# Kernel optimization log

Hardware: AMD Instinct MI355X
Metric: run time of the kernel (lower is better)

The kernel has to match this reference:

```python
import jax, jax.numpy as jnp
import numpy as np

D_MODEL = 4096
N_CHUNKS = 8
CHUNK = D_MODEL // N_CHUNKS
EPS = 1e-5


def setup_inputs() -> dict:
    key = jax.random.key(0)
    k = jax.random.split(key, 5)
    B, L = 4, 4096
    x = jax.random.normal(k[0], (B, L, D_MODEL), dtype=jnp.float32)
    # kaiming_uniform with a=sqrt(5) on [n,c,c]: fan_in = c, bound = 1/sqrt(fan_in)
    bound = 1.0 / np.sqrt(CHUNK)
    w1 = jax.random.uniform(k[1], (N_CHUNKS, CHUNK, CHUNK), jnp.float32, -bound, bound)
    w2 = jax.random.uniform(k[2], (N_CHUNKS, CHUNK, CHUNK), jnp.float32, -bound, bound)
    b1 = jnp.zeros((N_CHUNKS, CHUNK), jnp.float32)
    b2 = jnp.zeros((N_CHUNKS, CHUNK), jnp.float32)
    ln_g = jnp.ones((D_MODEL,), jnp.float32)
    ln_b = jnp.zeros((D_MODEL,), jnp.float32)
    return {"x": x, "w1": w1, "b1": b1, "w2": w2, "b2": b2, "ln_g": ln_g, "ln_b": ln_b}


def reference(x, w1, b1, w2, b2, ln_g, ln_b):
    B, L, d = x.shape
    xc = x.reshape(B, L, N_CHUNKS, CHUNK)
    h = jnp.einsum('blnc,ncd->blnd', xc, w1) + b1
    h = jax.nn.gelu(h, approximate=False)  # torch F.gelu default is exact erf
    h = jnp.einsum('blnc,ncd->blnd', h, w2) + b2
    out = h.reshape(B, L, d) + x  # dropout p=0.0 -> identity
    mu = jnp.mean(out, axis=-1, keepdims=True)
    var = jnp.var(out, axis=-1, keepdims=True)
    return (out - mu) * jax.lax.rsqrt(var + EPS) * ln_g + ln_b
```

## Files before the change

### kernel.cpp

```cpp
#include <hip/hip_runtime.h>
#include <hip/hip_bf16.h>

#define TOKENS 16384
#define DMODEL 4096
#define NCH 8
#define CH 512
#define BM 64

typedef short s16x8 __attribute__((ext_vector_type(8)));
typedef float f32x4 __attribute__((ext_vector_type(4)));

__device__ __forceinline__ unsigned short f2bf(float f) {
    unsigned u = __float_as_uint(f);
    u += 0x7fffu + ((u >> 16) & 1u);
    return (unsigned short)(u >> 16);
}

__device__ __forceinline__ float gelu_fast(float x) {
    float u = 1.5957691216057308f * x * (1.0f + 0.044715f * x * x);
    float e = __expf(u);
    return x - x * __builtin_amdgcn_rcpf(e + 1.0f);
}

__global__ __launch_bounds__(256)
void wprep_kernel(const float* __restrict__ w1, const float* __restrict__ w2,
                  unsigned short* __restrict__ p1, unsigned short* __restrict__ p2)
{
    const int lane = threadIdx.x;
    const int sub  = threadIdx.y;
    const int kt   = blockIdx.x;
    const int nb   = blockIdx.y * 4 + sub;
    const int which = blockIdx.z >> 3;
    const int n     = blockIdx.z & 7;

    const int kg  = lane >> 4;
    const int l15 = lane & 15;

    const float* src = (which ? w2 : w1) + (size_t)n * CH * CH;
    unsigned short* dst = (which ? p2 : p1) + (size_t)n * CH * CH
                        + ((size_t)(kt * 32 + nb) * 64 + lane) * 8;

    unsigned short v[8];
#pragma unroll
    for (int j = 0; j < 8; ++j)
        v[j] = f2bf(src[(size_t)(kt * 32 + kg * 8 + j) * CH + nb * 16 + l15]);

    uint4 q;
    q.x = (unsigned)v[0] | ((unsigned)v[1] << 16);
    q.y = (unsigned)v[2] | ((unsigned)v[3] << 16);
    q.z = (unsigned)v[4] | ((unsigned)v[5] << 16);
    q.w = (unsigned)v[6] | ((unsigned)v[7] << 16);
    *(uint4*)dst = q;
}

#define XC_BYTES (BM * CH * 2)
#define BBUF(i)  (XC_BYTES + (i) * 32768)

__global__ __launch_bounds__(512, 1)
void mlp_kernel(const float* __restrict__ x,
                const unsigned short* __restrict__ p1,
                const unsigned short* __restrict__ p2,
                const float* __restrict__ b1,
                const float* __restrict__ b2,
                float* __restrict__ mid)
{
    __shared__ unsigned char lds[XC_BYTES + 3 * 32768];
    const int tile = blockIdx.x;
    const int n    = blockIdx.y;
    const int tid  = threadIdx.x;
    const int wid  = tid >> 6;
    const int lane = tid & 63;
    const int row0 = tile * BM;
    const int kt0  = (tile >> 3) & 15;

    const unsigned short* p1n = p1 + (size_t)n * CH * CH;
    const unsigned short* p2n = p2 + (size_t)n * CH * CH;

    const int nwoff = wid * 64;
    const int l15   = lane & 15;
    const int kg    = lane >> 4;

    float b1v[4], b2v[4];
#pragma unroll
    for (int ni = 0; ni < 4; ++ni) {
        int col = n * CH + nwoff + ni * 16 + l15;
        b1v[ni] = b1[col];
        b2v[ni] = b2[col];
    }

    auto stageB = [&](const unsigned short* pk, int kt, int bufb) {
#pragma unroll
        for (int i = 0; i < 4; ++i) {
            const unsigned short* src = pk + ((size_t)(kt * 32 + wid * 4 + i) * 64 + lane) * 8;
            unsigned char* dstp = lds + bufb + (wid * 4 + i) * 1024;
            __builtin_amdgcn_global_load_lds(
                (const __attribute__((address_space(1))) void*)src,
                (__attribute__((address_space(3))) void*)dstp,
                16, 0, 0);
        }
    };

    stageB(p1n, kt0, BBUF(0));
    stageB(p1n, (kt0 + 1) & 15, BBUF(1));
    {
        const float* xc = x + (size_t)row0 * DMODEL + n * CH;
#pragma unroll
        for (int it = 0; it < 16; ++it) {
            int f = it * 512 + tid;
            int r = f >> 7;
            int c = (f & 127) << 2;
            const float4 v = *(const float4*)(xc + (size_t)r * DMODEL + c);
            unsigned lo = (unsigned)f2bf(v.x) | ((unsigned)f2bf(v.y) << 16);
            unsigned hi = (unsigned)f2bf(v.z) | ((unsigned)f2bf(v.w) << 16);
            int byte = ((r * CH + c) * 2) ^ ((r & 7) << 4);
            *(uint2*)(lds + byte) = make_uint2(lo, hi);
        }
    }
    __syncthreads();

    f32x4 acc[4][4];
    auto zacc = [&]() {
#pragma unroll
        for (int mi = 0; mi < 4; ++mi)
#pragma unroll
            for (int ni = 0; ni < 4; ++ni)
                acc[mi][ni] = (f32x4){0.f, 0.f, 0.f, 0.f};
    };

    auto step = [&](int kt, int bufb) {
        s16x8 a[4], b[4];
#pragma unroll
        for (int mi = 0; mi < 4; ++mi) {
            int r = mi * 16 + l15;
            int byte = ((r * CH + kt * 32 + kg * 8) * 2) ^ ((r & 7) << 4);
            a[mi] = *(const s16x8*)(lds + byte);
        }
#pragma unroll
        for (int ni = 0; ni < 4; ++ni)
            b[ni] = *(const s16x8*)(lds + bufb + ((wid * 4 + ni) * 64 + lane) * 16);
#pragma unroll
        for (int ni = 0; ni < 4; ++ni)
#pragma unroll
            for (int mi = 0; mi < 4; ++mi)
                acc[mi][ni] = __builtin_amdgcn_mfma_f32_16x16x32_bf16(
                    a[mi], b[ni], acc[mi][ni], 0, 0, 0);
    };

    zacc();
#pragma unroll
    for (int c = 0; c < 16; ++c) {
        if (c + 2 < 16) stageB(p1n, ((c + 2 + kt0) & 15), BBUF((c + 2) % 3));
        else            stageB(p2n, ((c + 2 - 16 + kt0) & 15), BBUF((c + 2) % 3));
        asm volatile("s_waitcnt vmcnt(8)" ::: "memory");
        step((c + kt0) & 15, BBUF(c % 3));
    }

    __syncthreads();

#pragma unroll
    for (int mi = 0; mi < 4; ++mi)
#pragma unroll
        for (int ni = 0; ni < 4; ++ni)
#pragma unroll
            for (int r = 0; r < 4; ++r) {
                float v = gelu_fast(acc[mi][ni][r] + b1v[ni]);
                int row  = mi * 16 + kg * 4 + r;
                int col  = nwoff + ni * 16 + l15;
                int byte = ((row * CH + col) * 2) ^ ((row & 7) << 4);
                *(unsigned short*)(lds + byte) = f2bf(v);
            }
    __syncthreads();

    zacc();
#pragma unroll
    for (int c = 16; c < 32; ++c) {
        if (c + 2 < 32) {
            stageB(p2n, ((c + 2 - 16 + kt0) & 15), BBUF((c + 2) % 3));
            asm volatile("s_waitcnt vmcnt(8)" ::: "memory");
        } else if (c == 30) {
            asm volatile("s_waitcnt vmcnt(4)" ::: "memory");
        } else {
            asm volatile("s_waitcnt vmcnt(0)" ::: "memory");
        }
        step(((c - 16) + kt0) & 15, BBUF(c % 3));
    }

    const float* xr = x   + (size_t)row0 * DMODEL + n * CH;
    float*       mr = mid + (size_t)row0 * DMODEL + n * CH;
#pragma unroll
    for (int mi = 0; mi < 4; ++mi)
#pragma unroll
        for (int ni = 0; ni < 4; ++ni)
#pragma unroll
            for (int r = 0; r < 4; ++r) {
                int row = mi * 16 + kg * 4 + r;
                int col = nwoff + ni * 16 + l15;
                float v = acc[mi][ni][r] + b2v[ni] + xr[(size_t)row * DMODEL + col];
                mr[(size_t)row * DMODEL + col] = v;
            }
}

__global__ __launch_bounds__(256)
void ln_kernel(float* __restrict__ out,
               const float* __restrict__ g,
               const float* __restrict__ bt)
{
    __shared__ float red[8];
    const int row = blockIdx.x;
    const int tid = threadIdx.x;
    float* p = out + (size_t)row * DMODEL;

    float4 v[4];
    float s = 0.f, ss = 0.f;
#pragma unroll
    for (int i = 0; i < 4; ++i) {
        v[i] = *(const float4*)(p + (i * 256 + tid) * 4);
        s  += v[i].x + v[i].y + v[i].z + v[i].w;
        ss += v[i].x * v[i].x + v[i].y * v[i].y + v[i].z * v[i].z + v[i].w * v[i].w;
    }
#pragma unroll
    for (int o = 32; o > 0; o >>= 1) {
        s  += __shfl_xor(s, o, 64);
        ss += __shfl_xor(ss, o, 64);
    }
    const int wid = tid >> 6, lane = tid & 63;
    if (lane == 0) { red[wid] = s; red[4 + wid] = ss; }
    __syncthreads();
    s  = red[0] + red[1] + red[2] + red[3];
    ss = red[4] + red[5] + red[6] + red[7];
    const float mu   = s * (1.f / DMODEL);
    const float var  = ss * (1.f / DMODEL) - mu * mu;
    const float rstd = rsqrtf(var + 1e-5f);

#pragma unroll
    for (int i = 0; i < 4; ++i) {
        int c = (i * 256 + tid) * 4;
        float4 gv = *(const float4*)(g + c);
        float4 bv = *(const float4*)(bt + c);
        float4 o;
        o.x = (v[i].x - mu) * rstd * gv.x + bv.x;
        o.y = (v[i].y - mu) * rstd * gv.y + bv.y;
        o.z = (v[i].z - mu) * rstd * gv.z + bv.z;
        o.w = (v[i].w - mu) * rstd * gv.w + bv.w;
        *(float4*)(p + c) = o;
    }
}

extern "C" void kernel_launch(void* const* d_in, const int* in_sizes, int n_in,
                              void* d_out, int out_size, void* d_ws, size_t ws_size,
                              hipStream_t stream)
{
    const float* x    = (const float*)d_in[0];
    const float* w1   = (const float*)d_in[1];
    const float* b1   = (const float*)d_in[2];
    const float* w2   = (const float*)d_in[3];
    const float* b2   = (const float*)d_in[4];
    const float* ln_g = (const float*)d_in[5];
    const float* ln_b = (const float*)d_in[6];
    float* out = (float*)d_out;

    unsigned short* p1 = (unsigned short*)d_ws;
    unsigned short* p2 = p1 + (size_t)NCH * CH * CH;

    wprep_kernel<<<dim3(16, 8, 16), dim3(64, 4), 0, stream>>>(w1, w2, p1, p2);
    mlp_kernel<<<dim3(TOKENS / BM, NCH), dim3(512), 0, stream>>>(x, p1, p2, b1, b2, out);
    ln_kernel<<<dim3(TOKENS), dim3(256), 0, stream>>>(out, ln_g, ln_b);
}
```

Measured before the change: 342.4 us.

## Enlarge MLP row tile to 96 with 2x4 wave grid and double-buffered weights

Raises the row tile from 64 to 96 tokens and arranges the 8 waves as a 2x4 grid, each computing a 48x128 output block (3x8 MFMA tiles), so each B fragment is reused across more rows. Weight staging drops from triple to double buffering with a barrier per k-step, which frees LDS for the larger activation tile. MFMA sections now run at raised priority via s_setprio, and bounds checks cover the ragged last tile (171 tiles). The trade-offs are more accumulator registers, a barrier on every step, and a shallower prefetch that may expose weight-load latency.

```diff
diff --git a/kernel.cpp b/kernel.cpp
--- a/kernel.cpp
+++ b/kernel.cpp
@@ -5,7 +5,8 @@
 #define DMODEL 4096
 #define NCH 8
 #define CH 512
-#define BM 64
+#define BM 96
+#define NTILES 171
 
 typedef short s16x8 __attribute__((ext_vector_type(8)));
 typedef float f32x4 __attribute__((ext_vector_type(4)));
@@ -64,7 +65,7 @@
                 const float* __restrict__ b2,
                 float* __restrict__ mid)
 {
-    __shared__ unsigned char lds[XC_BYTES + 3 * 32768];
+    __shared__ unsigned char lds[XC_BYTES + 2 * 32768];
     const int tile = blockIdx.x;
     const int n    = blockIdx.y;
     const int tid  = threadIdx.x;
@@ -73,17 +74,18 @@
     const int row0 = tile * BM;
     const int kt0  = (tile >> 3) & 15;
 
+    const int wg = wid >> 2;
+    const int wn = wid & 3;
+    const int l15 = lane & 15;
+    const int kg  = lane >> 4;
+
     const unsigned short* p1n = p1 + (size_t)n * CH * CH;
     const unsigned short* p2n = p2 + (size_t)n * CH * CH;
 
-    const int nwoff = wid * 64;
-    const int l15   = lane & 15;
-    const int kg    = lane >> 4;
-
-    float b1v[4], b2v[4];
-#pragma unroll
-    for (int ni = 0; ni < 4; ++ni) {
-        int col = n * CH + nwoff + ni * 16 + l15;
+    float b1v[8], b2v[8];
+#pragma unroll
+    for (int ni = 0; ni < 8; ++ni) {
+        int col = n * CH + wn * 128 + ni * 16 + l15;
         b1v[ni] = b1[col];
         b2v[ni] = b2[col];
     }
@@ -101,15 +103,16 @@
     };
 
     stageB(p1n, kt0, BBUF(0));
-    stageB(p1n, (kt0 + 1) & 15, BBUF(1));
     {
         const float* xc = x + (size_t)row0 * DMODEL + n * CH;
 #pragma unroll
-        for (int it = 0; it < 16; ++it) {
+        for (int it = 0; it < 24; ++it) {
             int f = it * 512 + tid;
             int r = f >> 7;
             int c = (f & 127) << 2;
-            const float4 v = *(const float4*)(xc + (size_t)r * DMODEL + c);
+            float4 v = make_float4(0.f, 0.f, 0.f, 0.f);
+            if (row0 + r < TOKENS)
+                v = *(const float4*)(xc + (size_t)r * DMODEL + c);
             unsigned lo = (unsigned)f2bf(v.x) | ((unsigned)f2bf(v.y) << 16);
             unsigned hi = (unsigned)f2bf(v.z) | ((unsigned)f2bf(v.w) << 16);
             int byte = ((r * CH + c) * 2) ^ ((r & 7) << 4);
@@ -118,85 +121,90 @@
     }
     __syncthreads();
 
-    f32x4 acc[4][4];
+    f32x4 acc[3][8];
     auto zacc = [&]() {
 #pragma unroll
-        for (int mi = 0; mi < 4; ++mi)
-#pragma unroll
-            for (int ni = 0; ni < 4; ++ni)
+        for (int mi = 0; mi < 3; ++mi)
+#pragma unroll
+            for (int ni = 0; ni < 8; ++ni)
                 acc[mi][ni] = (f32x4){0.f, 0.f, 0.f, 0.f};
     };
 
-    auto step = [&](int kt, int bufb) {
-        s16x8 a[4], b[4];
-#pragma unroll
-        for (int mi = 0; mi < 4; ++mi) {
-            int r = mi * 16 + l15;
-            int byte = ((r * CH + kt * 32 + kg * 8) * 2) ^ ((r & 7) << 4);
+    auto step = [&](int ktp, int bufb) {
+        s16x8 a[3], b[8];
+#pragma unroll
+        for (int mi = 0; mi < 3; ++mi) {
+            int r = wg * 48 + mi * 16 + l15;
+            int byte = ((r * CH + ktp * 32 + kg * 8) * 2) ^ ((r & 7) << 4);
             a[mi] = *(const s16x8*)(lds + byte);
         }
 #pragma unroll
-        for (int ni = 0; ni < 4; ++ni)
-            b[ni] = *(const s16x8*)(lds + bufb + ((wid * 4 + ni) * 64 + lane) * 16);
-#pragma unroll
-        for (int ni = 0; ni < 4; ++ni)
-#pragma unroll
-            for (int mi = 0; mi < 4; ++mi)
+        for (int ni = 0; ni < 8; ++ni)
+            b[ni] = *(const s16x8*)(lds + bufb + ((wn * 8 + ni) * 64 + lane) * 16);
+        __builtin_amdgcn_s_setprio(1);
+#pragma unroll
+        for (int ni = 0; ni < 8; ++ni)
+#pragma unroll
+            for (int mi = 0; mi < 3; ++mi)
                 acc[mi][ni] = __builtin_amdgcn_mfma_f32_16x16x32_bf16(
                     a[mi], b[ni], acc[mi][ni], 0, 0, 0);
+        __builtin_amdgcn_s_setprio(0);
     };
 
     zacc();
-#pragma unroll
+#pragma unroll 1
     for (int c = 0; c < 16; ++c) {
-        if (c + 2 < 16) stageB(p1n, ((c + 2 + kt0) & 15), BBUF((c + 2) % 3));
-        else            stageB(p2n, ((c + 2 - 16 + kt0) & 15), BBUF((c + 2) % 3));
-        asm volatile("s_waitcnt vmcnt(8)" ::: "memory");
-        step((c + kt0) & 15, BBUF(c % 3));
-    }
-
-    __syncthreads();
-
-#pragma unroll
-    for (int mi = 0; mi < 4; ++mi)
-#pragma unroll
-        for (int ni = 0; ni < 4; ++ni)
+        if (c < 15) stageB(p1n, (c + 1 + kt0) & 15, BBUF((c + 1) & 1));
+        else        stageB(p2n, kt0,                BBUF(0));
+        asm volatile("s_waitcnt vmcnt(4)" ::: "memory");
+        __builtin_amdgcn_s_barrier();
+        step((c + kt0) & 15, BBUF(c & 1));
+    }
+
+    __builtin_amdgcn_s_barrier();
+
+#pragma unroll
+    for (int mi = 0; mi < 3; ++mi)
+#pragma unroll
+        for (int ni = 0; ni < 8; ++ni)
 #pragma unroll
             for (int r = 0; r < 4; ++r) {
                 float v = gelu_fast(acc[mi][ni][r] + b1v[ni]);
-                int row  = mi * 16 + kg * 4 + r;
-                int col  = nwoff + ni * 16 + l15;
+                int row  = wg * 48 + mi * 16 + kg * 4 + r;
+                int col  = wn * 128 + ni * 16 + l15;
                 int byte = ((row * CH + col) * 2) ^ ((row & 7) << 4);
                 *(unsigned short*)(lds + byte) = f2bf(v);
             }
-    __syncthreads();
+    asm volatile("s_waitcnt lgkmcnt(0)" ::: "memory");
+    __builtin_amdgcn_s_barrier();
 
     zacc();
-#pragma unroll
-    for (int c = 16; c < 32; ++c) {
-        if (c + 2 < 32) {
-            stageB(p2n, ((c + 2 - 16 + kt0) & 15), BBUF((c + 2) % 3));
-            asm volatile("s_waitcnt vmcnt(8)" ::: "memory");
-        } else if (c == 30) {
+#pragma unroll 1
+    for (int cl = 0; cl < 16; ++cl) {
+        if (cl < 15) {
+            stageB(p2n, (cl + 1 + kt0) & 15, BBUF((cl + 1) & 1));
             asm volatile("s_waitcnt vmcnt(4)" ::: "memory");
         } else {
             asm volatile("s_waitcnt vmcnt(0)" ::: "memory");
         }
-        step(((c - 16) + kt0) & 15, BBUF(c % 3));
+        __builtin_amdgcn_s_barrier();
+        step((cl + kt0) & 15, BBUF(cl & 1));
     }
 
     const float* xr = x   + (size_t)row0 * DMODEL + n * CH;
     float*       mr = mid + (size_t)row0 * DMODEL + n * CH;
 #pragma unroll
-    for (int mi = 0; mi < 4; ++mi)
-#pragma unroll
-        for (int ni = 0; ni < 4; ++ni)
+    for (int mi = 0; mi < 3; ++mi)
+#pragma unroll
+        for (int ni = 0; ni < 8; ++ni)
 #pragma unroll
             for (int r = 0; r < 4; ++r) {
-                int row = mi * 16 + kg * 4 + r;
-                int col = nwoff + ni * 16 + l15;
-                float v = acc[mi][ni][r] + b2v[ni] + xr[(size_t)row * DMODEL + col];
-                mr[(size_t)row * DMODEL + col] = v;
+                int row = wg * 48 + mi * 16 + kg * 4 + r;
+                int col = wn * 128 + ni * 16 + l15;
+                if (row0 + row < TOKENS) {
+                    float v = acc[mi][ni][r] + b2v[ni] + xr[(size_t)row * DMODEL + col];
+                    mr[(size_t)row * DMODEL + col] = v;
+                }
             }
 }
 
@@ -263,6 +271,6 @@
     unsigned short* p2 = p1 + (size_t)NCH * CH * CH;
 
     wprep_kernel<<<dim3(16, 8, 16), dim3(64, 4), 0, stream>>>(w1, w2, p1, p2);
-    mlp_kernel<<<dim3(TOKENS / BM, NCH), dim3(512), 0, stream>>>(x, p1, p2, b1, b2, out);
+    mlp_kernel<<<dim3(NTILES, NCH), dim3(512), 0, stream>>>(x, p1, p2, b1, b2, out);
     ln_kernel<<<dim3(TOKENS), dim3(256), 0, stream>>>(out, ln_g, ln_b);
 }
```

Result: slower. 512.1 us (+49.6%).
